# Optimization experiments

Hardware: AMD Instinct MI355X
Metric: run time of the kernel (lower is better)

## Reference

```python
import jax, jax.numpy as jnp
import numpy as np

B, N, D, M = 32, 256, 3, 64
E_IN = 2 * D + 1  # 7: feats_i (3) + feats_j (3) + rel_dist (1)
E_HID = 2 * E_IN  # 14
N_HID = 2 * D     # 6
LN_EPS = 1e-5


def silu(x):
    return x * jax.nn.sigmoid(x)


def setup_inputs() -> dict:
    key = jax.random.key(0)
    ks = jax.random.split(key, 12)
    s = 0.05
    x = jax.random.normal(ks[0], (B, N, D), dtype=jnp.float32)
    mask = jax.random.randint(ks[1], (B, N), 0, 2) > 0
    # edge MLP: Linear(7->14), SiLU, Linear(14->64), SiLU
    W1 = jax.random.normal(ks[2], (E_IN, E_HID), jnp.float32) * s
    b1 = jnp.zeros((E_HID,), jnp.float32)
    W2 = jax.random.normal(ks[3], (E_HID, M), jnp.float32) * s
    b2 = jnp.zeros((M,), jnp.float32)
    # soft edge gate: Linear(64->1), Sigmoid
    Wg = jax.random.normal(ks[4], (M, 1), jnp.float32) * s
    bg = jnp.zeros((1,), jnp.float32)
    # node layernorm(3)
    gamma = jnp.ones((D,), jnp.float32)
    beta = jnp.zeros((D,), jnp.float32)
    # node MLP: Linear(67->6), SiLU, Linear(6->3)
    Wn1 = jax.random.normal(ks[5], (D + M, N_HID), jnp.float32) * s
    bn1 = jnp.zeros((N_HID,), jnp.float32)
    Wn2 = jax.random.normal(ks[6], (N_HID, D), jnp.float32) * s
    bn2 = jnp.zeros((D,), jnp.float32)
    return {"x": x, "W1": W1, "b1": b1, "W2": W2, "b2": b2,
            "Wg": Wg, "bg": bg, "gamma": gamma, "beta": beta,
            "Wn1": Wn1, "bn1": bn1, "Wn2": Wn2, "bn2": bn2, "mask": mask}


def reference(x, W1, b1, W2, b2, Wg, bg, gamma, beta, Wn1, bn1, Wn2, bn2, mask):
    b, n, d = x.shape
    # dense all-pairs relative coords & squared distance (feats == coors == x)
    rel = x[:, :, None, :] - x[:, None, :, :]              # [b, i, j, d]
    rel_dist = jnp.sum(rel * rel, axis=-1, keepdims=True)  # [b, i, j, 1]
    fi = jnp.broadcast_to(x[:, :, None, :], (b, n, n, d))
    fj = jnp.broadcast_to(x[:, None, :, :], (b, n, n, d))
    edge_in = jnp.concatenate([fi, fj, rel_dist], axis=-1)  # [b, i, j, 7]
    # edge MLP with SiLU after both linears
    h = silu(edge_in @ W1 + b1)                             # [b, i, j, 14]
    m_ij = silu(h @ W2 + b2)                                # [b, i, j, 64]
    # soft edge gating
    m_ij = m_ij * jax.nn.sigmoid(m_ij @ Wg + bg)
    # masked sum aggregation over j
    pair_mask = (mask[:, :, None] & mask[:, None, :])[..., None]
    m_ij = jnp.where(pair_mask, m_ij, 0.0)
    m_i = jnp.sum(m_ij, axis=2)                             # [b, i, 64]
    # feature layernorm on inputs to node MLP
    mu = jnp.mean(x, axis=-1, keepdims=True)
    var = jnp.var(x, axis=-1, keepdims=True)
    normed = (x - mu) * jax.lax.rsqrt(var + LN_EPS) * gamma + beta
    node_in = jnp.concatenate([normed, m_i], axis=-1)       # [b, n, 67]
    node_out = silu(node_in @ Wn1 + bn1) @ Wn2 + bn2 + x    # residual
    return node_out
```

## Files before the change

### kernel.cpp

```cpp
#include <hip/hip_runtime.h>

#define NN 256
#define EHID 14

typedef short short8 __attribute__((ext_vector_type(8)));
typedef float f32x16 __attribute__((ext_vector_type(16)));

__device__ __forceinline__ float sigm(float x) {
    return __builtin_amdgcn_rcpf(1.0f + __expf(-x));
}
__device__ __forceinline__ unsigned int bfbits(float f) {
    unsigned int u = __builtin_bit_cast(unsigned int, f);
    return (u + 0x7FFFu + ((u >> 16) & 1u)) >> 16;
}
__device__ __forceinline__ unsigned int cvtpk(float lo, float hi) {
    unsigned int r;
    asm("v_cvt_pk_bf16_f32 %0, %1, %2" : "=v"(r) : "v"(lo), "v"(hi));
    return r;
}
__device__ __forceinline__ short8 mk8(unsigned a, unsigned b, unsigned c, unsigned d) {
    int4 t = make_int4((int)a, (int)b, (int)c, (int)d);
    return __builtin_bit_cast(short8, t);
}

__global__ __launch_bounds__(256) void egnn_prep(
    const float* __restrict__ x,
    const float* __restrict__ gamma, const float* __restrict__ beta,
    const float* __restrict__ Wn1, const float* __restrict__ bn1,
    const float* __restrict__ Wn2, const float* __restrict__ bn2,
    const int* __restrict__ mask, float* __restrict__ out,
    int* __restrict__ cnt, int* __restrict__ list)
{
    const int b  = blockIdx.x;
    const int i  = threadIdx.x;
    const int gi = b * NN + i;
    const int l  = threadIdx.x & 63;
    const int m  = mask[gi];

    const unsigned long long mv = __ballot(m != 0);
    int base = 0;
    if (l == 0) base = atomicAdd(cnt, __popcll(mv));
    base = __shfl(base, 0, 64);
    const int prefix = __popcll(mv & ((1ull << l) - 1ull));

    if (m) {
        list[base + prefix] = gi;
    } else {
        const float xi0 = x[gi*3+0], xi1 = x[gi*3+1], xi2 = x[gi*3+2];
        const float mu  = (xi0 + xi1 + xi2) * (1.f/3.f);
        const float d0  = xi0 - mu, d1 = xi1 - mu, d2 = xi2 - mu;
        const float var = (d0*d0 + d1*d1 + d2*d2) * (1.f/3.f);
        const float rs  = rsqrtf(var + 1e-5f);
        const float n0  = d0*rs*gamma[0] + beta[0];
        const float n1  = d1*rs*gamma[1] + beta[1];
        const float n2  = d2*rs*gamma[2] + beta[2];
        float ss[6];
#pragma unroll
        for (int u = 0; u < 6; ++u) {
            const float sv = bn1[u] + n0*Wn1[u] + n1*Wn1[6+u] + n2*Wn1[12+u];
            ss[u] = sv * sigm(sv);
        }
#pragma unroll
        for (int c = 0; c < 3; ++c) {
            const float xres = (c == 0) ? xi0 : ((c == 1) ? xi1 : xi2);
            float sv = bn2[c] + xres;
#pragma unroll
            for (int u = 0; u < 6; ++u) sv += ss[u] * Wn2[u*3 + c];
            out[gi*3 + c] = sv;
        }
    }
}

__global__ __launch_bounds__(256) void egnn_edges(
    const float* __restrict__ x,
    const float* __restrict__ W1, const float* __restrict__ b1,
    const float* __restrict__ W2, const float* __restrict__ b2,
    const float* __restrict__ Wg, const float* __restrict__ bg,
    const float* __restrict__ gamma, const float* __restrict__ beta,
    const float* __restrict__ Wn1, const float* __restrict__ bn1,
    const float* __restrict__ Wn2, const float* __restrict__ bn2,
    const int* __restrict__ mask, float* __restrict__ out,
    const int* __restrict__ list, const int* __restrict__ cnt)
{
    const int l    = threadIdx.x & 63;
    const int l31  = l & 31;
    const int half = l >> 5;
    const int wgid = blockIdx.x * 4 + (threadIdx.x >> 6);
    const int NW   = gridDim.x * 4;

    unsigned a1p[4];
#pragma unroll
    for (int e2 = 0; e2 < 4; ++e2) {
        const int k0 = 8*half + 2*e2, k1 = k0 + 1;
        float w0 = 0.f, w1 = 0.f;
        if (l31 < EHID) {
            w0 = (k0 < 7) ? W1[k0*EHID + l31] : ((k0 == 7) ? b1[l31] : 0.f);
            w1 = (k1 < 7) ? W1[k1*EHID + l31] : ((k1 == 7) ? b1[l31] : 0.f);
        }
        a1p[e2] = bfbits(w0) | (bfbits(w1) << 16);
    }
    const short8 A1 = mk8(a1p[0], a1p[1], a1p[2], a1p[3]);

    unsigned a2p[2][4];
#pragma unroll
    for (int mf = 0; mf < 2; ++mf) {
        const int ch = l31 + 32*mf;
#pragma unroll
        for (int e2 = 0; e2 < 4; ++e2) {
            const int k0 = 8*half + 2*e2, k1 = k0 + 1;
            const float w0 = (k0 < EHID) ? W2[k0*64 + ch] : ((k0 == EHID) ? b2[ch] : 0.f);
            const float w1 = (k1 < EHID) ? W2[k1*64 + ch] : ((k1 == EHID) ? b2[ch] : 0.f);
            a2p[mf][e2] = bfbits(w0) | (bfbits(w1) << 16);
        }
    }
    const short8 A20 = mk8(a2p[0][0], a2p[0][1], a2p[0][2], a2p[0][3]);
    const short8 A21 = mk8(a2p[1][0], a2p[1][1], a2p[1][2], a2p[1][3]);

    float wgv0[16], wgv1[16];
#pragma unroll
    for (int r = 0; r < 16; ++r) {
        const int row = (r & 3) + 8*(r >> 2) + 4*half;
        wgv0[r] = Wg[row];
        wgv1[r] = Wg[row + 32];
    }
    const float bg0 = bg[0];
    const int total = cnt[0];

    for (int ii = wgid; ii < total; ii += NW) {
        const int gi = list[ii];
        const int b  = gi >> 8;
        const int i  = gi & 255;
        const float* xb = x + b * (NN * 3);
        const float xi0 = xb[i*3+0], xi1 = xb[i*3+1], xi2 = xb[i*3+2];

        unsigned long long mb[4];
#pragma unroll
        for (int t = 0; t < 4; ++t)
            mb[t] = __ballot(mask[b*NN + t*64 + l] != 0);

        float macc0[16], macc1[16];
#pragma unroll
        for (int r = 0; r < 16; ++r) { macc0[r] = 0.f; macc1[r] = 0.f; }

#pragma unroll 2
        for (int rnd = 0; rnd < 8; ++rnd) {
            const int e = rnd*32 + l31;
            const float xj0 = xb[e*3+0], xj1 = xb[e*3+1], xj2 = xb[e*3+2];
            const float r0 = xi0-xj0, r1 = xi1-xj1, r2 = xi2-xj2;
            const float rd = r0*r0 + r1*r1 + r2*r2;
            const unsigned p0 = cvtpk(xi0, xi1);
            const unsigned p1 = cvtpk(xi2, xj0);
            const unsigned p2 = cvtpk(xj1, xj2);
            const unsigned p3 = cvtpk(rd, 1.0f);
            const short8 B1 = mk8(p0, p1, p2, p3);

            f32x16 zc;
#pragma unroll
            for (int r = 0; r < 16; ++r) zc[r] = 0.f;
            const f32x16 c = __builtin_amdgcn_mfma_f32_32x32x16_bf16(A1, B1, zc, 0, 0, 0);

            float s[8];
#pragma unroll
            for (int r = 0; r < 8; ++r) s[r] = c[r] * sigm(c[r]);
            const unsigned q01 = cvtpk(s[0], s[1]);
            const unsigned q23 = cvtpk(s[2], s[3]);
            const unsigned q45 = cvtpk(s[4], s[5]);
            const unsigned q67 = cvtpk(s[6], s[7]);
            const unsigned sendA = half ? q01 : q45;
            const unsigned sendB = half ? q23 : q67;
            const unsigned recvA = (unsigned)__shfl_xor((int)sendA, 32, 64);
            const unsigned recvB = (unsigned)__shfl_xor((int)sendB, 32, 64);
            const unsigned w0 = half ? recvA : q01;
            const unsigned w1 = half ? recvB : q23;
            const unsigned w2 = half ? q45   : recvA;
            const unsigned w3 = half ? 0x00003F80u : recvB;
            const short8 B2 = mk8(w0, w1, w2, w3);

            const f32x16 c0 = __builtin_amdgcn_mfma_f32_32x32x16_bf16(A20, B2, zc, 0, 0, 0);
            const f32x16 c1 = __builtin_amdgcn_mfma_f32_32x32x16_bf16(A21, B2, zc, 0, 0, 0);

            float v0[16], v1[16];
            float gp = 0.f;
#pragma unroll
            for (int r = 0; r < 16; ++r) {
                v0[r] = c0[r] * sigm(c0[r]);
                gp += v0[r] * wgv0[r];
                v1[r] = c1[r] * sigm(c1[r]);
                gp += v1[r] * wgv1[r];
            }
            const float go = __shfl_xor(gp, 32, 64);
            float g = sigm(gp + go + bg0);
            const unsigned mhw = (unsigned)(mb[rnd >> 1] >> ((rnd & 1) * 32));
            g = ((mhw >> l31) & 1u) ? g : 0.f;
#pragma unroll
            for (int r = 0; r < 16; ++r) {
                macc0[r] += v0[r] * g;
                macc1[r] += v1[r] * g;
            }
        }

        float pn[6];
#pragma unroll
        for (int u = 0; u < 6; ++u) pn[u] = 0.f;
#pragma unroll
        for (int r = 0; r < 16; ++r) {
            const int row = (r & 3) + 8*(r >> 2) + 4*half;
            const float m0 = macc0[r], m1 = macc1[r];
            const float* wr0 = Wn1 + (3 + row) * 6;
            const float* wr1 = Wn1 + (3 + row + 32) * 6;
#pragma unroll
            for (int u = 0; u < 6; ++u) pn[u] += m0 * wr0[u] + m1 * wr1[u];
        }
#pragma unroll
        for (int sft = 1; sft <= 32; sft <<= 1) {
#pragma unroll
            for (int u = 0; u < 6; ++u) pn[u] += __shfl_xor(pn[u], sft, 64);
        }

        const float mu  = (xi0 + xi1 + xi2) * (1.f/3.f);
        const float d0  = xi0 - mu, d1 = xi1 - mu, d2 = xi2 - mu;
        const float var = (d0*d0 + d1*d1 + d2*d2) * (1.f/3.f);
        const float rs  = rsqrtf(var + 1e-5f);
        const float n0  = d0*rs*gamma[0] + beta[0];
        const float n1  = d1*rs*gamma[1] + beta[1];
        const float n2  = d2*rs*gamma[2] + beta[2];
        float ss[6];
#pragma unroll
        for (int u = 0; u < 6; ++u) {
            const float sv = pn[u] + bn1[u] + n0*Wn1[u] + n1*Wn1[6+u] + n2*Wn1[12+u];
            ss[u] = sv * sigm(sv);
        }
        if (l < 3) {
            const float xres = (l == 0) ? xi0 : ((l == 1) ? xi1 : xi2);
            float sv = bn2[l] + xres;
#pragma unroll
            for (int u = 0; u < 6; ++u) sv += ss[u] * Wn2[u*3 + l];
            out[gi*3 + l] = sv;
        }
    }
}

extern "C" void kernel_launch(void* const* d_in, const int* in_sizes, int n_in,
                              void* d_out, int out_size, void* d_ws, size_t ws_size,
                              hipStream_t stream) {
    (void)in_sizes; (void)n_in; (void)out_size; (void)ws_size;
    const float* x     = (const float*)d_in[0];
    const float* W1    = (const float*)d_in[1];
    const float* b1    = (const float*)d_in[2];
    const float* W2    = (const float*)d_in[3];
    const float* b2    = (const float*)d_in[4];
    const float* Wg    = (const float*)d_in[5];
    const float* bg    = (const float*)d_in[6];
    const float* gamma = (const float*)d_in[7];
    const float* beta  = (const float*)d_in[8];
    const float* Wn1   = (const float*)d_in[9];
    const float* bn1   = (const float*)d_in[10];
    const float* Wn2   = (const float*)d_in[11];
    const float* bn2   = (const float*)d_in[12];
    const int*   mask  = (const int*)d_in[13];
    float* out = (float*)d_out;

    int* cnt  = (int*)d_ws;
    int* list = (int*)d_ws + 16;

    hipMemsetAsync(cnt, 0, sizeof(int), stream);
    hipLaunchKernelGGL(egnn_prep, dim3(32), dim3(256), 0, stream,
                       x, gamma, beta, Wn1, bn1, Wn2, bn2, mask, out, cnt, list);
    hipLaunchKernelGGL(egnn_edges, dim3(1024), dim3(256), 0, stream,
                       x, W1, b1, W2, b2, Wg, bg, gamma, beta,
                       Wn1, bn1, Wn2, bn2, mask, out, list, cnt);
}
```

Baseline: 55.65 us.

## Compact masked j-nodes per batch so edge loop only processes valid neighbors

The prep kernel now also builds a per-batch compacted list of masked-in node indices and a per-batch count. The edge kernel iterates only over ceil(count/32) rounds of valid j nodes, gathering x via the index list, instead of all 8 rounds with a mask test. It also hoists loop invariants (zero accumulator, packed xi pair) and splits the gate dot-product into four partial sums to shorten the dependency chain. This adds an indirect load per round and a shared-memory barrier in prep.

```diff
diff --git a/kernel.cpp b/kernel.cpp
--- a/kernel.cpp
+++ b/kernel.cpp
@@ -29,22 +29,38 @@
     const float* __restrict__ Wn1, const float* __restrict__ bn1,
     const float* __restrict__ Wn2, const float* __restrict__ bn2,
     const int* __restrict__ mask, float* __restrict__ out,
-    int* __restrict__ cnt, int* __restrict__ list)
+    int* __restrict__ icnt, int* __restrict__ ilist,
+    int* __restrict__ jcnt, int* __restrict__ jlist)
 {
-    const int b  = blockIdx.x;
-    const int i  = threadIdx.x;
-    const int gi = b * NN + i;
-    const int l  = threadIdx.x & 63;
-    const int m  = mask[gi];
-
-    const unsigned long long mv = __ballot(m != 0);
-    int base = 0;
-    if (l == 0) base = atomicAdd(cnt, __popcll(mv));
-    base = __shfl(base, 0, 64);
-    const int prefix = __popcll(mv & ((1ull << l) - 1ull));
-
+    __shared__ unsigned long long wbal[4];
+    const int b   = blockIdx.x;
+    const int tid = threadIdx.x;
+    const int w   = tid >> 6;
+    const int l   = tid & 63;
+    const int gi  = b * NN + tid;
+    const int m   = mask[gi];
+
+    const unsigned long long ball = __ballot(m != 0);
+    if (l == 0) wbal[w] = ball;
+    __syncthreads();
+
+    int jbase = 0;
+#pragma unroll
+    for (int t = 0; t < 4; ++t) if (t < w) jbase += __popcll(wbal[t]);
+    const int prefix = __popcll(ball & ((1ull << l) - 1ull));
+    if (m) jlist[b * NN + jbase + prefix] = tid;
+    if (tid == 0) {
+        int s = 0;
+#pragma unroll
+        for (int t = 0; t < 4; ++t) s += __popcll(wbal[t]);
+        jcnt[b] = s;
+    }
+
+    int ibase = 0;
+    if (l == 0) ibase = atomicAdd(icnt, __popcll(ball));
+    ibase = __shfl(ibase, 0, 64);
     if (m) {
-        list[base + prefix] = gi;
+        ilist[ibase + prefix] = gi;
     } else {
         const float xi0 = x[gi*3+0], xi1 = x[gi*3+1], xi2 = x[gi*3+2];
         const float mu  = (xi0 + xi1 + xi2) * (1.f/3.f);
@@ -79,8 +95,9 @@
     const float* __restrict__ gamma, const float* __restrict__ beta,
     const float* __restrict__ Wn1, const float* __restrict__ bn1,
     const float* __restrict__ Wn2, const float* __restrict__ bn2,
-    const int* __restrict__ mask, float* __restrict__ out,
-    const int* __restrict__ list, const int* __restrict__ cnt)
+    float* __restrict__ out,
+    const int* __restrict__ ilist, const int* __restrict__ icnt,
+    const int* __restrict__ jcnt, const int* __restrict__ jlist)
 {
     const int l    = threadIdx.x & 63;
     const int l31  = l & 31;
@@ -124,39 +141,40 @@
         wgv1[r] = Wg[row + 32];
     }
     const float bg0 = bg[0];
-    const int total = cnt[0];
+    const int total = icnt[0];
+
+    f32x16 zc;
+#pragma unroll
+    for (int r = 0; r < 16; ++r) zc[r] = 0.f;
 
     for (int ii = wgid; ii < total; ii += NW) {
-        const int gi = list[ii];
+        const int gi = ilist[ii];
         const int b  = gi >> 8;
         const int i  = gi & 255;
         const float* xb = x + b * (NN * 3);
+        const int*   jb = jlist + b * NN;
         const float xi0 = xb[i*3+0], xi1 = xb[i*3+1], xi2 = xb[i*3+2];
-
-        unsigned long long mb[4];
-#pragma unroll
-        for (int t = 0; t < 4; ++t)
-            mb[t] = __ballot(mask[b*NN + t*64 + l] != 0);
+        const int jc = jcnt[b];
+        const int rounds = (jc + 31) >> 5;
+
+        const unsigned p0 = cvtpk(xi0, xi1);
 
         float macc0[16], macc1[16];
 #pragma unroll
         for (int r = 0; r < 16; ++r) { macc0[r] = 0.f; macc1[r] = 0.f; }
 
-#pragma unroll 2
-        for (int rnd = 0; rnd < 8; ++rnd) {
-            const int e = rnd*32 + l31;
-            const float xj0 = xb[e*3+0], xj1 = xb[e*3+1], xj2 = xb[e*3+2];
+        for (int rnd = 0; rnd < rounds; ++rnd) {
+            const int eidx  = rnd*32 + l31;
+            const int valid = eidx < jc;
+            const int jl    = jb[valid ? eidx : 0];
+            const float xj0 = xb[jl*3+0], xj1 = xb[jl*3+1], xj2 = xb[jl*3+2];
             const float r0 = xi0-xj0, r1 = xi1-xj1, r2 = xi2-xj2;
             const float rd = r0*r0 + r1*r1 + r2*r2;
-            const unsigned p0 = cvtpk(xi0, xi1);
             const unsigned p1 = cvtpk(xi2, xj0);
             const unsigned p2 = cvtpk(xj1, xj2);
             const unsigned p3 = cvtpk(rd, 1.0f);
             const short8 B1 = mk8(p0, p1, p2, p3);
 
-            f32x16 zc;
-#pragma unroll
-            for (int r = 0; r < 16; ++r) zc[r] = 0.f;
             const f32x16 c = __builtin_amdgcn_mfma_f32_32x32x16_bf16(A1, B1, zc, 0, 0, 0);
 
             float s[8];
@@ -180,18 +198,18 @@
             const f32x16 c1 = __builtin_amdgcn_mfma_f32_32x32x16_bf16(A21, B2, zc, 0, 0, 0);
 
             float v0[16], v1[16];
-            float gp = 0.f;
+            float gpa = 0.f, gpb = 0.f, gpc = 0.f, gpd = 0.f;
 #pragma unroll
             for (int r = 0; r < 16; ++r) {
                 v0[r] = c0[r] * sigm(c0[r]);
-                gp += v0[r] * wgv0[r];
                 v1[r] = c1[r] * sigm(c1[r]);
-                gp += v1[r] * wgv1[r];
+                if (r < 8) { gpa += v0[r] * wgv0[r]; gpc += v1[r] * wgv1[r]; }
+                else       { gpb += v0[r] * wgv0[r]; gpd += v1[r] * wgv1[r]; }
             }
+            const float gp = (gpa + gpb) + (gpc + gpd);
             const float go = __shfl_xor(gp, 32, 64);
             float g = sigm(gp + go + bg0);
-            const unsigned mhw = (unsigned)(mb[rnd >> 1] >> ((rnd & 1) * 32));
-            g = ((mhw >> l31) & 1u) ? g : 0.f;
+            g = valid ? g : 0.f;
 #pragma unroll
             for (int r = 0; r < 16; ++r) {
                 macc0[r] += v0[r] * g;
@@ -260,13 +278,16 @@
     const int*   mask  = (const int*)d_in[13];
     float* out = (float*)d_out;
 
-    int* cnt  = (int*)d_ws;
-    int* list = (int*)d_ws + 16;
-
-    hipMemsetAsync(cnt, 0, sizeof(int), stream);
+    int* icnt  = (int*)d_ws;
+    int* jcnt  = (int*)((char*)d_ws + 256);
+    int* ilist = (int*)((char*)d_ws + 4096);
+    int* jlist = (int*)((char*)d_ws + 65536);
+
+    hipMemsetAsync(icnt, 0, sizeof(int), stream);
     hipLaunchKernelGGL(egnn_prep, dim3(32), dim3(256), 0, stream,
-                       x, gamma, beta, Wn1, bn1, Wn2, bn2, mask, out, cnt, list);
+                       x, gamma, beta, Wn1, bn1, Wn2, bn2, mask, out,
+                       icnt, ilist, jcnt, jlist);
     hipLaunchKernelGGL(egnn_edges, dim3(1024), dim3(256), 0, stream,
                        x, W1, b1, W2, b2, Wg, bg, gamma, beta,
-                       Wn1, bn1, Wn2, bn2, mask, out, list, cnt);
-}
+                       Wn1, bn1, Wn2, bn2, out, ilist, icnt, jcnt, jlist);
+}
```

Measured after the change: 59.36 us. +6.7%, slower.
